# Optimization experiments

Hardware: AMD Instinct MI355X
Metric: run time of the kernel (lower is better)

Reference implementation:

```python
import jax, jax.numpy as jnp
import numpy as np

N = 100000          # nodes
E = 1600000         # edges (avg degree 16)
DIN = 6             # len(keys)
D = 64              # hidden/out dim
L = 4               # num_layers
SELF_DEG = 16       # fixed out-degree of self_node (node 0)


def setup_inputs() -> dict:
    key = jax.random.key(0)
    ks = jax.random.split(key, 13)
    s = 0.1
    x = jax.random.normal(ks[0], (N, DIN), jnp.float32)
    # edges: force first SELF_DEG edges to originate at node 0; all other
    # sources drawn from [1, N) so node 0 has exactly SELF_DEG neighbors.
    src = jax.random.randint(ks[1], (E,), 1, N, dtype=jnp.int32)
    src = src.at[:SELF_DEG].set(0)
    dst = jax.random.randint(ks[2], (E,), 0, N, dtype=jnp.int32)
    edge_index = jnp.stack([src, dst], axis=0)
    return {
        'x': x,
        'edge_index': edge_index,
        'self_node': 0,
        'W0l': jax.random.normal(ks[3], (DIN, D), jnp.float32) * s,
        'W0r': jax.random.normal(ks[4], (DIN, D), jnp.float32) * s,
        'b0': jnp.zeros((D,), jnp.float32),
        'Wl': jax.random.normal(ks[5], (L - 1, D, D), jnp.float32) * s,
        'Wr': jax.random.normal(ks[6], (L - 1, D, D), jnp.float32) * s,
        'b': jnp.zeros((L - 1, D), jnp.float32),
        'Wlog': jax.random.normal(ks[7], (2 * D, 1), jnp.float32) * s,
        'blog': jnp.zeros((1,), jnp.float32),
        'Wval': jax.random.normal(ks[8], (D, 1), jnp.float32) * s,
        'bval': jnp.zeros((1,), jnp.float32),
    }


def _sage_layer(h, src, dst, Wl, Wr, b):
    # SAGEConv (mean aggr, root_weight=True): lin_l(mean_{j->i} x_j) + lin_r(x_i) + bias
    msgs = h[src]                                   # [E, d] gather
    agg = jax.ops.segment_sum(msgs, dst, num_segments=N)
    cnt = jax.ops.segment_sum(jnp.ones((src.shape[0],), h.dtype), dst, num_segments=N)
    mean = agg / jnp.maximum(cnt, 1.0)[:, None]
    return mean @ Wl + h @ Wr + b


def reference(x, edge_index, self_node, W0l, W0r, b0, Wl, Wr, b, Wlog, blog, Wval, bval):
    src, dst = edge_index[0], edge_index[1]
    # GraphSAGE backbone: ReLU between layers, none after the last (eval: no dropout)
    h = jax.nn.relu(_sage_layer(x, src, dst, W0l, W0r, b0))
    for i in range(L - 1):
        h = _sage_layer(h, src, dst, Wl[i], Wr[i], b[i])
        if i < L - 2:
            h = jax.nn.relu(h)
    self_emb = h[self_node]                         # [D]
    # neighbors of self_node: edges with src == self_node (fixed count SELF_DEG)
    nbr_edge = jnp.nonzero(src == self_node, size=SELF_DEG, fill_value=0)[0]
    neighbors = dst[nbr_edge]                       # [SELF_DEG]
    edge_emb = jnp.concatenate(
        [jnp.broadcast_to(self_emb, (SELF_DEG, D)), h[neighbors]], axis=-1)  # [SELF_DEG, 2D]
    logits = (edge_emb @ Wlog + blog)[:, 0]         # [SELF_DEG]
    value = (self_emb @ Wval + bval)[0]             # scalar
    return logits, value, neighbors
```

## Files before the change

kernel.cpp:

```cpp
#include <hip/hip_runtime.h>

#define DHID 64
#define DIN 6
#define SDEG 16
#define BSH 6
#define NBMAX 2048
#define NGRP 128

static __device__ __forceinline__ float rlane(float v, int k) {
  return __uint_as_float(__builtin_amdgcn_readlane(__float_as_uint(v), k));
}
static __device__ __forceinline__ unsigned short f2bf(float f) {
  unsigned u = __float_as_uint(f);
  return (unsigned short)((u + 0x7fff + ((u >> 16) & 1)) >> 16);
}
static __device__ __forceinline__ float bf2f(unsigned short u) {
  return __uint_as_float((unsigned)u << 16);
}
static __device__ __forceinline__ float bflo(unsigned u) {
  return __uint_as_float(u << 16);
}
static __device__ __forceinline__ float bfhi(unsigned u) {
  return __uint_as_float(u & 0xffff0000u);
}


__global__ __launch_bounds__(256) void k_hist2(const int* __restrict__ dst,
                                               int* __restrict__ hist, int E, int NB) {
  __shared__ int h[NBMAX];
  int g = blockIdx.x;
  for (int i = threadIdx.x; i < NB; i += 256) h[i] = 0;
  __syncthreads();
  int chunk = (E + NGRP - 1) / NGRP;
  int e0 = g * chunk, e1 = min(E, e0 + chunk);
  for (int e = e0 + threadIdx.x; e < e1; e += 256)
    atomicAdd(&h[dst[e] >> BSH], 1);
  __syncthreads();
  for (int i = threadIdx.x; i < NB; i += 256)
    hist[(size_t)g * NB + i] = h[i];
}

__global__ __launch_bounds__(256) void k_scan2a(int* __restrict__ hist,
                                                int* __restrict__ colsum, int NB) {
  int b = blockIdx.x * 256 + threadIdx.x;
  if (b >= NB) return;
  int s = 0;
  for (int g = 0; g < NGRP; ++g) {
    size_t idx = (size_t)g * NB + b;
    int v = hist[idx];
    hist[idx] = s;
    s += v;
  }
  colsum[b] = s;
}

__global__ void k_scan2b(const int* __restrict__ colsum, int* __restrict__ bbase,
                         int NB) {
  int t = threadIdx.x;
  int run = 0;
  for (int base = 0; base < NB; base += 64) {
    int i = base + t;
    int d = (i < NB) ? colsum[i] : 0;
    int v = d;
#pragma unroll
    for (int off = 1; off < 64; off <<= 1) {
      int u = __shfl_up(v, off);
      if (t >= off) v += u;
    }
    if (i < NB) bbase[i] = run + v - d;
    run += __shfl(v, 63);
  }
  if (t == 0) bbase[NB] = run;
}

__global__ __launch_bounds__(256) void k_scatter2(
    const int* __restrict__ src, const int* __restrict__ dst,
    const int* __restrict__ hist, const int* __restrict__ bbase,
    int* __restrict__ ebuf, const int* __restrict__ selfp,
    int* __restrict__ selfcnt, int* __restrict__ selflist, int E, int NB) {
  __shared__ int cur[NBMAX];
  int g = blockIdx.x;
  for (int i = threadIdx.x; i < NB; i += 256)
    cur[i] = hist[(size_t)g * NB + i] + bbase[i];
  __syncthreads();
  int self = *selfp;
  int chunk = (E + NGRP - 1) / NGRP;
  int e0 = g * chunk, e1 = min(E, e0 + chunk);
  for (int e = e0 + threadIdx.x; e < e1; e += 256) {
    int s = src[e], d = dst[e];
    int pos = atomicAdd(&cur[d >> BSH], 1);
    ebuf[pos] = (s << BSH) | (d & 63);
    if (s == self) {
      int i = atomicAdd(selfcnt, 1);
      if (i < SDEG) selflist[i] = e;
    }
  }
}

__global__ __launch_bounds__(256) void k_bfill(
    const int* __restrict__ ebuf, const int* __restrict__ bbase,
    int* __restrict__ rowptr, int* __restrict__ deg, int* __restrict__ col,
    int N) {
  __shared__ int cnt[64], cur[64];
  int b = blockIdx.x;
  int t = threadIdx.x;
  if (t < 64) cnt[t] = 0;
  __syncthreads();
  int lo = bbase[b], hi = bbase[b + 1];
  for (int i = lo + t; i < hi; i += 256) atomicAdd(&cnt[ebuf[i] & 63], 1);
  __syncthreads();
  if (t < 64) {
    int c = cnt[t];
    int v = c;
#pragma unroll
    for (int off = 1; off < 64; off <<= 1) {
      int u = __shfl_up(v, off);
      if (t >= off) v += u;
    }
    int start = lo + v - c;
    int node = (b << BSH) + t;
    if (node < N) { rowptr[node] = start; deg[node] = c; }
    cur[t] = start;
  }
  __syncthreads();
  for (int i = lo + t; i < hi; i += 256) {
    int p = ebuf[i];
    int pos = atomicAdd(&cur[p & 63], 1);
    col[pos] = p >> BSH;
  }
}


__global__ __launch_bounds__(256) void k_layer0(
    const float* __restrict__ x, const int* __restrict__ rowptr,
    const int* __restrict__ deg, const int* __restrict__ col,
    const float* __restrict__ W0l, const float* __restrict__ W0r,
    const float* __restrict__ b0, unsigned short* __restrict__ hbout, int N) {
  int lane = threadIdx.x & 63;
  int wid = blockIdx.x * (blockDim.x >> 6) + (threadIdx.x >> 6);
  int nw = gridDim.x * (blockDim.x >> 6);
  float w0l[DIN], w0r[DIN];
#pragma unroll
  for (int k = 0; k < DIN; ++k) {
    w0l[k] = W0l[k * DHID + lane];
    w0r[k] = W0r[k * DHID + lane];
  }
  float bv = b0[lane];
  int d6 = (lane < DIN) ? lane : 0;
  for (int node = wid; node < N; node += nw) {
    int start = rowptr[node], cnt = deg[node];
    float a0 = 0.f, a1 = 0.f, a2 = 0.f, a3 = 0.f;
    float a4 = 0.f, a5 = 0.f, a6 = 0.f, a7 = 0.f;
    int e = 0;
    for (; e + 8 <= cnt; e += 8) {
      int s0 = col[start + e + 0], s1 = col[start + e + 1];
      int s2 = col[start + e + 2], s3 = col[start + e + 3];
      int s4 = col[start + e + 4], s5 = col[start + e + 5];
      int s6 = col[start + e + 6], s7 = col[start + e + 7];
      a0 += x[s0 * DIN + d6];
      a1 += x[s1 * DIN + d6];
      a2 += x[s2 * DIN + d6];
      a3 += x[s3 * DIN + d6];
      a4 += x[s4 * DIN + d6];
      a5 += x[s5 * DIN + d6];
      a6 += x[s6 * DIN + d6];
      a7 += x[s7 * DIN + d6];
    }
    for (; e < cnt; ++e) a0 += x[col[start + e] * DIN + d6];
    float acc = ((a0 + a1) + (a2 + a3)) + ((a4 + a5) + (a6 + a7));
    float mean = acc / fmaxf((float)cnt, 1.0f);
    float xi = x[node * DIN + d6];
    float outv = bv;
#pragma unroll
    for (int k = 0; k < DIN; ++k) {
      outv = fmaf(rlane(mean, k), w0l[k], outv);
      outv = fmaf(rlane(xi, k), w0r[k], outv);
    }
    outv = fmaxf(outv, 0.f);
    hbout[(size_t)node * DHID + lane] = f2bf(outv);
  }
}


__global__ __launch_bounds__(256) void k_agg(
    const unsigned short* __restrict__ hb, const int* __restrict__ rowptr,
    const int* __restrict__ deg, const int* __restrict__ col,
    unsigned short* __restrict__ meanb, int N) {
  int lane = threadIdx.x & 63;
  int wid = blockIdx.x * (blockDim.x >> 6) + (threadIdx.x >> 6);
  int nw = gridDim.x * (blockDim.x >> 6);
  for (int node = wid; node < N; node += nw) {
    int start = rowptr[node], cnt = deg[node];
    float a0 = 0.f, a1 = 0.f, a2 = 0.f, a3 = 0.f;
    float a4 = 0.f, a5 = 0.f, a6 = 0.f, a7 = 0.f;
    int e = 0;
    for (; e + 8 <= cnt; e += 8) {
      int s0 = col[start + e + 0], s1 = col[start + e + 1];
      int s2 = col[start + e + 2], s3 = col[start + e + 3];
      int s4 = col[start + e + 4], s5 = col[start + e + 5];
      int s6 = col[start + e + 6], s7 = col[start + e + 7];
      a0 += bf2f(hb[(size_t)s0 * DHID + lane]);
      a1 += bf2f(hb[(size_t)s1 * DHID + lane]);
      a2 += bf2f(hb[(size_t)s2 * DHID + lane]);
      a3 += bf2f(hb[(size_t)s3 * DHID + lane]);
      a4 += bf2f(hb[(size_t)s4 * DHID + lane]);
      a5 += bf2f(hb[(size_t)s5 * DHID + lane]);
      a6 += bf2f(hb[(size_t)s6 * DHID + lane]);
      a7 += bf2f(hb[(size_t)s7 * DHID + lane]);
    }
    for (; e < cnt; ++e) a0 += bf2f(hb[(size_t)col[start + e] * DHID + lane]);
    float s = ((a0 + a1) + (a2 + a3)) + ((a4 + a5) + (a6 + a7));
    meanb[(size_t)node * DHID + lane] = f2bf(s / fmaxf((float)cnt, 1.0f));
  }
}


__global__ __launch_bounds__(256, 2) void k_mm(
    const unsigned short* __restrict__ meanb,
    const unsigned short* __restrict__ hinb,
    const float* __restrict__ Wl, const float* __restrict__ Wr,
    const float* __restrict__ b, float* __restrict__ hout,
    unsigned short* __restrict__ hbout, int N, int do_relu) {
  __shared__ float4 sW[2064];
  int t = threadIdx.x;
  const float4* wl4 = (const float4*)Wl;
  const float4* wr4 = (const float4*)Wr;
  for (int i = t; i < 1024; i += 256) sW[i] = wl4[i];
  for (int i = t; i < 1024; i += 256) sW[1024 + i] = wr4[i];
  if (t < 16) sW[2048 + t] = ((const float4*)b)[t];
  __syncthreads();

  int node = blockIdx.x * 256 + t;
  if (node >= N) return;

  const uint4* m4 = (const uint4*)(meanb + (size_t)node * DHID);
  const uint4* h4 = (const uint4*)(hinb + (size_t)node * DHID);

  float acc[DHID];
#pragma unroll
  for (int jc = 0; jc < 16; ++jc) {
    float4 bv = sW[2048 + jc];
    acc[jc * 4 + 0] = bv.x; acc[jc * 4 + 1] = bv.y;
    acc[jc * 4 + 2] = bv.z; acc[jc * 4 + 3] = bv.w;
  }

  for (int kc = 0; kc < 8; ++kc) {
    uint4 mv = m4[kc];
    uint4 hv = h4[kc];
    float am[8], ah[8];
    am[0] = bflo(mv.x); am[1] = bfhi(mv.x);
    am[2] = bflo(mv.y); am[3] = bfhi(mv.y);
    am[4] = bflo(mv.z); am[5] = bfhi(mv.z);
    am[6] = bflo(mv.w); am[7] = bfhi(mv.w);
    ah[0] = bflo(hv.x); ah[1] = bfhi(hv.x);
    ah[2] = bflo(hv.y); ah[3] = bfhi(hv.y);
    ah[4] = bflo(hv.z); ah[5] = bfhi(hv.z);
    ah[6] = bflo(hv.w); ah[7] = bfhi(hv.w);
#pragma unroll
    for (int kk = 0; kk < 8; ++kk) {
      int k = kc * 8 + kk;
      float a = am[kk], hh = ah[kk];
#pragma unroll
      for (int jc = 0; jc < 16; ++jc) {
        float4 wlv = sW[k * 16 + jc];
        float4 wrv = sW[1024 + k * 16 + jc];
        acc[jc * 4 + 0] = fmaf(a, wlv.x, fmaf(hh, wrv.x, acc[jc * 4 + 0]));
        acc[jc * 4 + 1] = fmaf(a, wlv.y, fmaf(hh, wrv.y, acc[jc * 4 + 1]));
        acc[jc * 4 + 2] = fmaf(a, wlv.z, fmaf(hh, wrv.z, acc[jc * 4 + 2]));
        acc[jc * 4 + 3] = fmaf(a, wlv.w, fmaf(hh, wrv.w, acc[jc * 4 + 3]));
      }
    }
  }

#pragma unroll
  for (int jc = 0; jc < 16; ++jc) {
    if (do_relu) {
      acc[jc * 4 + 0] = fmaxf(acc[jc * 4 + 0], 0.f);
      acc[jc * 4 + 1] = fmaxf(acc[jc * 4 + 1], 0.f);
      acc[jc * 4 + 2] = fmaxf(acc[jc * 4 + 2], 0.f);
      acc[jc * 4 + 3] = fmaxf(acc[jc * 4 + 3], 0.f);
    }
  }
  if (hout) {
    float4* o4 = (float4*)(hout + (size_t)node * DHID);
#pragma unroll
    for (int jc = 0; jc < 16; ++jc) {
      float4 v;
      v.x = acc[jc * 4 + 0]; v.y = acc[jc * 4 + 1];
      v.z = acc[jc * 4 + 2]; v.w = acc[jc * 4 + 3];
      o4[jc] = v;
    }
  }
  if (hbout) {
    ushort4* ob = (ushort4*)(hbout + (size_t)node * DHID);
#pragma unroll
    for (int jc = 0; jc < 16; ++jc) {
      ushort4 bvu;
      bvu.x = f2bf(acc[jc * 4 + 0]); bvu.y = f2bf(acc[jc * 4 + 1]);
      bvu.z = f2bf(acc[jc * 4 + 2]); bvu.w = f2bf(acc[jc * 4 + 3]);
      ob[jc] = bvu;
    }
  }
}


__global__ void k_head(const float* __restrict__ h, const int* __restrict__ dst,
                       const int* __restrict__ selfp, const int* __restrict__ selflist,
                       const int* __restrict__ selfcnt, const float* __restrict__ Wlog,
                       const float* __restrict__ blog, const float* __restrict__ Wval,
                       const float* __restrict__ bval, float* __restrict__ out) {
  __shared__ int sorted[SDEG];
  __shared__ int nbr[SDEG];
  int t = threadIdx.x;
  int self = *selfp;
  if (t == 0) {
    int c = *selfcnt;
    if (c > SDEG) c = SDEG;
    int tmp[SDEG];
    for (int j = 0; j < SDEG; ++j) tmp[j] = (j < c) ? selflist[j] : 0;
    for (int a = 1; a < c; ++a) {
      int v = tmp[a];
      int bq = a - 1;
      while (bq >= 0 && tmp[bq] > v) { tmp[bq + 1] = tmp[bq]; --bq; }
      tmp[bq + 1] = v;
    }
    for (int j = 0; j < SDEG; ++j) sorted[j] = tmp[j];
  }
  __syncthreads();
  if (t < SDEG) nbr[t] = dst[sorted[t]];
  __syncthreads();

  int r = t >> 2, p = t & 3;
  float part = 0.f;
  for (int k = p * 32; k < p * 32 + 32; ++k) {
    float ev = (k < DHID) ? h[self * DHID + k] : h[nbr[r] * DHID + (k - DHID)];
    part += ev * Wlog[k];
  }
  part += __shfl_xor(part, 1);
  part += __shfl_xor(part, 2);
  if (p == 0) out[r] = part + blog[0];

  float pv = h[self * DHID + t] * Wval[t];
#pragma unroll
  for (int off = 32; off; off >>= 1) pv += __shfl_xor(pv, off);
  if (t == 0) out[SDEG] = pv + bval[0];

  if (t < SDEG) out[SDEG + 1 + t] = (float)nbr[t];
}


extern "C" void kernel_launch(void* const* d_in, const int* in_sizes, int n_in,
                              void* d_out, int out_size, void* d_ws, size_t ws_size,
                              hipStream_t stream) {
  const float* x    = (const float*)d_in[0];
  const int*   ei   = (const int*)d_in[1];
  const int*   selfp= (const int*)d_in[2];
  const float* W0l  = (const float*)d_in[3];
  const float* W0r  = (const float*)d_in[4];
  const float* b0   = (const float*)d_in[5];
  const float* Wl   = (const float*)d_in[6];
  const float* Wr   = (const float*)d_in[7];
  const float* bb   = (const float*)d_in[8];
  const float* Wlog = (const float*)d_in[9];
  const float* blog = (const float*)d_in[10];
  const float* Wval = (const float*)d_in[11];
  const float* bval = (const float*)d_in[12];
  float* out = (float*)d_out;

  int N = in_sizes[0] / DIN;
  int E = in_sizes[1] / 2;
  int NB = (N + 63) >> BSH;
  const int* src = ei;
  const int* dstp = ei + E;

  size_t off = 0;
  auto alloc = [&](size_t bytes) {
    void* p = (char*)d_ws + off;
    off += (bytes + 255) & ~(size_t)255;
    return p;
  };
  int* meta    = (int*)alloc(64 * 4);
  int* hist    = (int*)alloc((size_t)NGRP * NB * 4);
  int* bbase   = (int*)alloc((size_t)(NB + 1) * 4);
  int* colsum  = (int*)alloc((size_t)NB * 4);
  int* ebuf    = (int*)alloc((size_t)E * 4);
  int* deg     = (int*)alloc((size_t)N * 4);
  int* rowptr  = (int*)alloc((size_t)N * 4);
  int* col     = (int*)alloc((size_t)E * 4);
  float* hF    = (float*)alloc((size_t)N * DHID * 4);
  unsigned short* mb  = (unsigned short*)alloc((size_t)N * DHID * 2);
  unsigned short* hb0 = (unsigned short*)alloc((size_t)N * DHID * 2);
  unsigned short* hb1 = (unsigned short*)alloc((size_t)N * DHID * 2);
  unsigned short* hb2 = (unsigned short*)alloc((size_t)N * DHID * 2);
  int* selfcnt  = meta + 0;
  int* selflist = meta + 1;

  hipMemsetAsync(meta, 0, 64 * 4, stream);

  const int TB = 256;
  k_hist2<<<NGRP, TB, 0, stream>>>(dstp, hist, E, NB);
  k_scan2a<<<(NB + TB - 1) / TB, TB, 0, stream>>>(hist, colsum, NB);
  k_scan2b<<<1, 64, 0, stream>>>(colsum, bbase, NB);
  k_scatter2<<<NGRP, TB, 0, stream>>>(src, dstp, hist, bbase, ebuf, selfp,
                                      selfcnt, selflist, E, NB);
  k_bfill<<<NB, TB, 0, stream>>>(ebuf, bbase, rowptr, deg, col, N);

  k_layer0<<<2048, 256, 0, stream>>>(x, rowptr, deg, col, W0l, W0r, b0, hb0, N);

  int mm_grid = (N + 255) / 256;
  k_agg<<<2048, 256, 0, stream>>>(hb0, rowptr, deg, col, mb, N);
  k_mm<<<mm_grid, 256, 0, stream>>>(mb, hb0, Wl + 0 * 4096, Wr + 0 * 4096,
                                    bb + 0 * 64, (float*)nullptr, hb1, N, 1);
  k_agg<<<2048, 256, 0, stream>>>(hb1, rowptr, deg, col, mb, N);
  k_mm<<<mm_grid, 256, 0, stream>>>(mb, hb1, Wl + 1 * 4096, Wr + 1 * 4096,
                                    bb + 1 * 64, (float*)nullptr, hb2, N, 1);
  k_agg<<<2048, 256, 0, stream>>>(hb2, rowptr, deg, col, mb, N);
  k_mm<<<mm_grid, 256, 0, stream>>>(mb, hb2, Wl + 2 * 4096, Wr + 2 * 4096,
                                    bb + 2 * 64, hF, (unsigned short*)nullptr, N, 0);

  k_head<<<1, 64, 0, stream>>>(hF, dstp, selfp, selflist, selfcnt, Wlog, blog,
                               Wval, bval, out);
}
```

Measured before the change: 517.7 us.

## Split wavefront lanes across edges in gather kernels with shuffle reduction

```diff
diff --git a/kernel.cpp b/kernel.cpp
--- a/kernel.cpp
+++ b/kernel.cpp
@@ -137,6 +137,8 @@
     const float* __restrict__ W0l, const float* __restrict__ W0r,
     const float* __restrict__ b0, unsigned short* __restrict__ hbout, int N) {
   int lane = threadIdx.x & 63;
+  int eg = lane >> 3;
+  int d8 = lane & 7;
   int wid = blockIdx.x * (blockDim.x >> 6) + (threadIdx.x >> 6);
   int nw = gridDim.x * (blockDim.x >> 6);
   float w0l[DIN], w0r[DIN];
@@ -149,27 +151,30 @@
   int d6 = (lane < DIN) ? lane : 0;
   for (int node = wid; node < N; node += nw) {
     int start = rowptr[node], cnt = deg[node];
-    float a0 = 0.f, a1 = 0.f, a2 = 0.f, a3 = 0.f;
-    float a4 = 0.f, a5 = 0.f, a6 = 0.f, a7 = 0.f;
+    float a = 0.f, a2 = 0.f;
     int e = 0;
-    for (; e + 8 <= cnt; e += 8) {
-      int s0 = col[start + e + 0], s1 = col[start + e + 1];
-      int s2 = col[start + e + 2], s3 = col[start + e + 3];
-      int s4 = col[start + e + 4], s5 = col[start + e + 5];
-      int s6 = col[start + e + 6], s7 = col[start + e + 7];
-      a0 += x[s0 * DIN + d6];
-      a1 += x[s1 * DIN + d6];
-      a2 += x[s2 * DIN + d6];
-      a3 += x[s3 * DIN + d6];
-      a4 += x[s4 * DIN + d6];
-      a5 += x[s5 * DIN + d6];
-      a6 += x[s6 * DIN + d6];
-      a7 += x[s7 * DIN + d6];
-    }
-    for (; e < cnt; ++e) a0 += x[col[start + e] * DIN + d6];
-    float acc = ((a0 + a1) + (a2 + a3)) + ((a4 + a5) + (a6 + a7));
-    float mean = acc / fmaxf((float)cnt, 1.0f);
-    float xi = x[node * DIN + d6];
+    for (; e + 16 <= cnt; e += 16) {
+      int s0 = col[start + e + eg];
+      int s1 = col[start + e + 8 + eg];
+      a  += (d8 < DIN) ? x[(size_t)s0 * DIN + d8] : 0.f;
+      a2 += (d8 < DIN) ? x[(size_t)s1 * DIN + d8] : 0.f;
+    }
+    if (e + 8 <= cnt) {
+      int s = col[start + e + eg];
+      a += (d8 < DIN) ? x[(size_t)s * DIN + d8] : 0.f;
+      e += 8;
+    }
+    int rem = cnt - e;
+    if (eg < rem) {
+      int s = col[start + e + eg];
+      a += (d8 < DIN) ? x[(size_t)s * DIN + d8] : 0.f;
+    }
+    a += a2;
+    a += __shfl_xor(a, 8);
+    a += __shfl_xor(a, 16);
+    a += __shfl_xor(a, 32);
+    float mean = a / fmaxf((float)cnt, 1.0f);
+    float xi = x[(size_t)node * DIN + d6];
     float outv = bv;
 #pragma unroll
     for (int k = 0; k < DIN; ++k) {
@@ -187,30 +192,52 @@
     const int* __restrict__ deg, const int* __restrict__ col,
     unsigned short* __restrict__ meanb, int N) {
   int lane = threadIdx.x & 63;
+  int qg = lane >> 4;
+  int l16 = lane & 15;
+  const uint2* hw = (const uint2*)hb;
   int wid = blockIdx.x * (blockDim.x >> 6) + (threadIdx.x >> 6);
   int nw = gridDim.x * (blockDim.x >> 6);
   for (int node = wid; node < N; node += nw) {
     int start = rowptr[node], cnt = deg[node];
     float a0 = 0.f, a1 = 0.f, a2 = 0.f, a3 = 0.f;
-    float a4 = 0.f, a5 = 0.f, a6 = 0.f, a7 = 0.f;
+    float b0 = 0.f, b1 = 0.f, b2 = 0.f, b3 = 0.f;
     int e = 0;
     for (; e + 8 <= cnt; e += 8) {
-      int s0 = col[start + e + 0], s1 = col[start + e + 1];
-      int s2 = col[start + e + 2], s3 = col[start + e + 3];
-      int s4 = col[start + e + 4], s5 = col[start + e + 5];
-      int s6 = col[start + e + 6], s7 = col[start + e + 7];
-      a0 += bf2f(hb[(size_t)s0 * DHID + lane]);
-      a1 += bf2f(hb[(size_t)s1 * DHID + lane]);
-      a2 += bf2f(hb[(size_t)s2 * DHID + lane]);
-      a3 += bf2f(hb[(size_t)s3 * DHID + lane]);
-      a4 += bf2f(hb[(size_t)s4 * DHID + lane]);
-      a5 += bf2f(hb[(size_t)s5 * DHID + lane]);
-      a6 += bf2f(hb[(size_t)s6 * DHID + lane]);
-      a7 += bf2f(hb[(size_t)s7 * DHID + lane]);
-    }
-    for (; e < cnt; ++e) a0 += bf2f(hb[(size_t)col[start + e] * DHID + lane]);
-    float s = ((a0 + a1) + (a2 + a3)) + ((a4 + a5) + (a6 + a7));
-    meanb[(size_t)node * DHID + lane] = f2bf(s / fmaxf((float)cnt, 1.0f));
+      int s0 = col[start + e + qg];
+      int s1 = col[start + e + 4 + qg];
+      uint2 u0 = hw[(size_t)s0 * 16 + l16];
+      uint2 u1 = hw[(size_t)s1 * 16 + l16];
+      a0 += bflo(u0.x); a1 += bfhi(u0.x);
+      a2 += bflo(u0.y); a3 += bfhi(u0.y);
+      b0 += bflo(u1.x); b1 += bfhi(u1.x);
+      b2 += bflo(u1.y); b3 += bfhi(u1.y);
+    }
+    if (e + 4 <= cnt) {
+      int s = col[start + e + qg];
+      uint2 u = hw[(size_t)s * 16 + l16];
+      a0 += bflo(u.x); a1 += bfhi(u.x);
+      a2 += bflo(u.y); a3 += bfhi(u.y);
+      e += 4;
+    }
+    int rem = cnt - e;
+    if (qg < rem) {
+      int s = col[start + e + qg];
+      uint2 u = hw[(size_t)s * 16 + l16];
+      b0 += bflo(u.x); b1 += bfhi(u.x);
+      b2 += bflo(u.y); b3 += bfhi(u.y);
+    }
+    a0 += b0; a1 += b1; a2 += b2; a3 += b3;
+    a0 += __shfl_xor(a0, 16); a0 += __shfl_xor(a0, 32);
+    a1 += __shfl_xor(a1, 16); a1 += __shfl_xor(a1, 32);
+    a2 += __shfl_xor(a2, 16); a2 += __shfl_xor(a2, 32);
+    a3 += __shfl_xor(a3, 16); a3 += __shfl_xor(a3, 32);
+    if (qg == 0) {
+      float inv = 1.0f / fmaxf((float)cnt, 1.0f);
+      uint2 o;
+      o.x = (unsigned)f2bf(a0 * inv) | ((unsigned)f2bf(a1 * inv) << 16);
+      o.y = (unsigned)f2bf(a2 * inv) | ((unsigned)f2bf(a3 * inv) << 16);
+      ((uint2*)meanb)[(size_t)node * 16 + l16] = o;
+    }
   }
 }
 
```

Result: faster. 434.1 us (-16.1%).
